# Performance work log

Hardware: AMD Instinct MI355X
Metric: run time of the kernel (lower is better)

## Reference

```python
import jax, jax.numpy as jnp
import numpy as np

NUM_HEADS = 12

def setup_inputs() -> dict:
    key = jax.random.key(0)
    ks = jax.random.split(key, 9)
    B, N, C = 4, 1024, 768
    hd = C // NUM_HEADS  # 64
    return {
        "x": jax.random.normal(ks[0], (B, N, C), dtype=jnp.float32),
        "prev_attn": jax.random.uniform(ks[1], (B, NUM_HEADS, N, N), dtype=jnp.float32) / N,
        "qkv_w": jax.random.normal(ks[2], (3 * C, C), dtype=jnp.float32) * 0.02,
        "proj_w": jax.random.normal(ks[3], (C, C), dtype=jnp.float32) * 0.02,
        "proj_b": jax.random.normal(ks[4], (C,), dtype=jnp.float32) * 0.02,
        "bp_w1": jax.random.normal(ks[5], (hd // 2, 2 * hd), dtype=jnp.float32) * 0.02,
        "bp_b1": jax.random.normal(ks[6], (hd // 2,), dtype=jnp.float32) * 0.02,
        "bp_w2": jax.random.normal(ks[7], (3, hd // 2), dtype=jnp.float32) * 0.02,
        "bp_b2": jax.random.normal(ks[8], (3,), dtype=jnp.float32) * 0.02,
    }

def reference(x, prev_attn, qkv_w, proj_w, proj_b, bp_w1, bp_b1, bp_w2, bp_b2):
    B, N, C = x.shape
    H = NUM_HEADS
    hd = C // H
    scale = hd ** -0.5
    # qkv projection: [B,N,3C] -> [3,B,H,N,hd]
    qkv = (x @ qkv_w.T).reshape(B, N, 3, H, hd).transpose(2, 0, 3, 1, 4)
    q, k, v = qkv[0], qkv[1], qkv[2]
    # scaled dot-product scores [B,H,N,N]
    attn_logits = jnp.einsum('bhnd,bhmd->bhnm', q, k) * scale
    cur_attn = jax.nn.softmax(attn_logits, axis=-1)
    # per-(b,h,n) bias MLP on concat(q,k): [B,H,N,2*hd] -> [B,H,N,3]
    qk = jnp.concatenate((q, k), axis=-1)
    h1 = jax.nn.relu(jnp.einsum('bhnd,od->bhno', qk, bp_w1) + bp_b1)
    bias = jnp.abs(jnp.einsum('bhno,po->bhnp', h1, bp_w2) + bp_b2)  # [B,H,N,3]
    # blend current attention, previous attention, and uniform term
    attn = (cur_attn * (1.0 + bias[..., 0:1])
            + prev_attn * bias[..., 1:2]
            - bias[..., 2:3] / N)
    out = jnp.einsum('bhnm,bhmd->bhnd', attn, v)  # [B,H,N,hd]
    out = out.transpose(0, 2, 1, 3).reshape(B, N, C)
    out = out @ proj_w.T + proj_b
    return (out, cur_attn)
```

## Files before the change

kernel.cpp:

```cpp
#include <hip/hip_runtime.h>

typedef __bf16 bf16_t;
typedef __bf16 bf16x8 __attribute__((ext_vector_type(8)));
typedef __bf16 bf16x4 __attribute__((ext_vector_type(4)));
typedef float f32x4 __attribute__((ext_vector_type(4)));

static constexpr int Bb = 4, Hh = 12, Nn = 1024, Cc = 768, HD = 64;
static constexpr int OUT0 = Bb * Nn * Cc;

#define GLD16(gp, lp)                                                       \
  __builtin_amdgcn_global_load_lds(                                         \
      (const __attribute__((address_space(1))) unsigned int*)(gp),          \
      (__attribute__((address_space(3))) unsigned int*)(lp), 16, 0, 0)

__global__ __launch_bounds__(256) void convert_all(
    const float* __restrict__ x, const float* __restrict__ qw, const float* __restrict__ pw,
    bf16_t* __restrict__ xb, bf16_t* __restrict__ qwb, bf16_t* __restrict__ pwb) {
  const int NX = (Bb * Nn * Cc) / 4;
  const int NQ = (3 * Cc * Cc) / 4;
  int i = blockIdx.x * 256 + threadIdx.x;
  const float4* src;
  bf16_t* dst;
  int off;
  if (i < NX) { src = (const float4*)x; dst = xb; off = i; }
  else if (i < NX + NQ) { src = (const float4*)qw; dst = qwb; off = i - NX; }
  else { src = (const float4*)pw; dst = pwb; off = i - NX - NQ; }
  float4 v = src[off];
  bf16x4 o;
  o[0] = (bf16_t)v.x; o[1] = (bf16_t)v.y; o[2] = (bf16_t)v.z; o[3] = (bf16_t)v.w;
  *(bf16x4*)(dst + (size_t)off * 4) = o;
}

__global__ __launch_bounds__(256) void gemm_qkv(
    const bf16_t* __restrict__ A, const bf16_t* __restrict__ Bm,
    bf16_t* __restrict__ q_bf, bf16_t* __restrict__ k_bf, bf16_t* __restrict__ vT_bf) {
  __shared__ bf16_t As[128 * 32];
  __shared__ bf16_t Bs[128 * 32];
  const int tid = threadIdx.x;
  const int lane = tid & 63;
  const int w = tid >> 6;
  const int wr = w >> 1, wc = w & 1;
  const int g = lane >> 4, r = lane & 15;
  const int m0 = (blockIdx.x / 18) << 7;
  const int n0 = (blockIdx.x % 18) << 7;

  const f32x4 fz = {0.f, 0.f, 0.f, 0.f};
  f32x4 acc[4][4];
#pragma unroll
  for (int i = 0; i < 4; i++)
#pragma unroll
    for (int j = 0; j < 4; j++) acc[i][j] = fz;

  for (int k0 = 0; k0 < 768; k0 += 32) {
#pragma unroll
    for (int c = 0; c < 2; c++) {
      int row = w * 32 + c * 16 + (lane >> 2);
      int kof = (lane & 3) << 3;
      GLD16(&A[(size_t)(m0 + row) * 768 + k0 + kof], (char*)As + w * 2048 + c * 1024);
      GLD16(&Bm[(size_t)(n0 + row) * 768 + k0 + kof], (char*)Bs + w * 2048 + c * 1024);
    }
    __syncthreads();
    bf16x8 af[4], bfv[4];
#pragma unroll
    for (int i = 0; i < 4; i++) af[i] = *(const bf16x8*)&As[(wr * 64 + i * 16 + r) * 32 + g * 8];
#pragma unroll
    for (int j = 0; j < 4; j++) bfv[j] = *(const bf16x8*)&Bs[(wc * 64 + j * 16 + r) * 32 + g * 8];
#pragma unroll
    for (int i = 0; i < 4; i++)
#pragma unroll
      for (int j = 0; j < 4; j++)
        acc[i][j] = __builtin_amdgcn_mfma_f32_16x16x32_bf16(af[i], bfv[j], acc[i][j], 0, 0, 0);
    __syncthreads();
  }

#pragma unroll
  for (int i = 0; i < 4; i++) {
#pragma unroll
    for (int j = 0; j < 4; j++) {
      int c = n0 + wc * 64 + j * 16 + r;
#pragma unroll
      for (int e = 0; e < 4; e++) {
        int mrow = m0 + wr * 64 + i * 16 + g * 4 + e;
        float val = acc[i][j][e];
        int which = c / 768;
        int cc = c - which * 768;
        int h = cc >> 6, d = cc & 63;
        int b = mrow >> 10, n = mrow & 1023;
        size_t bh = (size_t)(b * Hh + h);
        if (which == 0)      q_bf[(bh * Nn + n) * HD + d] = (bf16_t)val;
        else if (which == 1) k_bf[(bh * Nn + n) * HD + d] = (bf16_t)val;
        else                 vT_bf[(bh * HD + d) * Nn + n] = (bf16_t)val;
      }
    }
  }
}

__global__ __launch_bounds__(256) void gemm_proj64(
    const bf16_t* __restrict__ A, const bf16_t* __restrict__ Bm,
    float* __restrict__ outF, const float* __restrict__ bias) {
  __shared__ bf16_t As[64 * 40];
  __shared__ bf16_t Bs[128 * 40];
  const int tid = threadIdx.x, lane = tid & 63, w = tid >> 6;
  const int wr = w >> 1, wc = w & 1;
  const int g = lane >> 4, r = lane & 15;
  const int m0 = (blockIdx.x / 6) << 6;
  const int n0 = (blockIdx.x % 6) << 7;
  const f32x4 fz = {0.f, 0.f, 0.f, 0.f};
  f32x4 acc[2][4];
#pragma unroll
  for (int i = 0; i < 2; i++)
#pragma unroll
    for (int j = 0; j < 4; j++) acc[i][j] = fz;

  for (int k0 = 0; k0 < 768; k0 += 32) {
    {
      int row = tid >> 2, kof = (tid & 3) << 3;
      *(bf16x8*)&As[row * 40 + kof] = *(const bf16x8*)&A[(size_t)(m0 + row) * 768 + k0 + kof];
    }
#pragma unroll
    for (int p = 0; p < 2; p++) {
      int idx = tid + (p << 8);
      int row = idx >> 2, kof = (idx & 3) << 3;
      *(bf16x8*)&Bs[row * 40 + kof] = *(const bf16x8*)&Bm[(size_t)(n0 + row) * 768 + k0 + kof];
    }
    __syncthreads();
    bf16x8 af[2], bfv[4];
#pragma unroll
    for (int i = 0; i < 2; i++) af[i] = *(const bf16x8*)&As[(wr * 32 + i * 16 + r) * 40 + g * 8];
#pragma unroll
    for (int j = 0; j < 4; j++) bfv[j] = *(const bf16x8*)&Bs[(wc * 64 + j * 16 + r) * 40 + g * 8];
#pragma unroll
    for (int i = 0; i < 2; i++)
#pragma unroll
      for (int j = 0; j < 4; j++)
        acc[i][j] = __builtin_amdgcn_mfma_f32_16x16x32_bf16(af[i], bfv[j], acc[i][j], 0, 0, 0);
    __syncthreads();
  }

#pragma unroll
  for (int i = 0; i < 2; i++)
#pragma unroll
    for (int j = 0; j < 4; j++) {
      int c = n0 + wc * 64 + j * 16 + r;
#pragma unroll
      for (int e = 0; e < 4; e++) {
        int mrow = m0 + wr * 32 + i * 16 + g * 4 + e;
        outF[(size_t)mrow * 768 + c] = acc[i][j][e] + bias[c];
      }
    }
}

__global__ __launch_bounds__(256) void bias_mlp(
    const bf16_t* __restrict__ qb, const bf16_t* __restrict__ kb,
    const float* __restrict__ w1, const float* __restrict__ b1,
    const float* __restrict__ w2, const float* __restrict__ b2,
    float* __restrict__ bias4) {
  __shared__ float w1s[32 * 130];
  __shared__ float qks[8][128];
  __shared__ float h1s[8][32];
  const int t = threadIdx.x;
#pragma unroll
  for (int p = 0; p < 16; p++) {
    int idx = p * 256 + t;
    w1s[(idx >> 7) * 130 + (idx & 127)] = w1[idx];
  }
  const int rl = t >> 5, u = t & 31;
  const float b1u = b1[u];
  for (int ro = 0; ro < 4; ro++) {
    const int rowg = blockIdx.x * 32 + ro * 8 + rl;
    {
      int i4 = u * 4;
      const bf16_t* src = (i4 < 64) ? (qb + (size_t)rowg * HD + i4)
                                    : (kb + (size_t)rowg * HD + (i4 - 64));
      bf16x4 vv = *(const bf16x4*)src;
#pragma unroll
      for (int z = 0; z < 4; z++) qks[rl][i4 + z] = (float)vv[z];
    }
    __syncthreads();
    float accv = b1u;
#pragma unroll 16
    for (int i2 = 0; i2 < 64; i2++) {
      float2 wv = *(const float2*)&w1s[u * 130 + i2 * 2];
      float2 qv = *(const float2*)&qks[rl][i2 * 2];
      accv += wv.x * qv.x + wv.y * qv.y;
    }
    h1s[rl][u] = fmaxf(accv, 0.f);
    __syncthreads();
    if (u < 4) {
      float outv = 0.f;
      if (u < 3) {
        float s = b2[u];
#pragma unroll
        for (int j = 0; j < 32; j++) s += w2[u * 32 + j] * h1s[rl][j];
        float v = fabsf(s);
        outv = (u == 0) ? (1.f + v) : ((u == 1) ? v : -v * (1.f / (float)Nn));
      }
      bias4[(size_t)rowg * 4 + u] = outv;
    }
    __syncthreads();
  }
}

__global__ __launch_bounds__(256, 2) void attn_fused(
    const bf16_t* __restrict__ qb, const bf16_t* __restrict__ kb,
    const bf16_t* __restrict__ vT, const float* __restrict__ prev,
    const float* __restrict__ bias4, float* __restrict__ cur,
    bf16_t* __restrict__ oh) {
  __shared__ char Plb[32 * 2048];
  __shared__ float redsum[32][4];
  const int bid = blockIdx.x;
  const int tile = (bid & 7) * 192 + (bid >> 3);
  const int bh = tile >> 5, mt = tile & 31;
  const int tid = threadIdx.x;
  const int lane = tid & 63, w = tid >> 6;
  const int g = lane >> 4, r = lane & 15;
  const int row0 = mt << 5;
  const int cbase = w << 8;

  const bf16_t* qp = qb + ((size_t)bh * Nn + row0) * HD;
  const bf16_t* kp = kb + (size_t)bh * Nn * HD;
  const float* ppr0 = prev + (size_t)bh * Nn * Nn + (size_t)(row0 + r) * Nn + cbase + (g << 2);
  char* myPrev = Plb + (w << 14);
  bf16x8 q00 = *(const bf16x8*)&qp[r * HD + g * 8];
  bf16x8 q01 = *(const bf16x8*)&qp[r * HD + g * 8 + 32];
  bf16x8 q10 = *(const bf16x8*)&qp[(16 + r) * HD + g * 8];
  bf16x8 q11 = *(const bf16x8*)&qp[(16 + r) * HD + g * 8 + 32];
  bf16x8 qa0, qa1, qb0, qb1;
#pragma unroll
  for (int j = 0; j < 8; j++) {
    qa0[j] = (bf16_t)((float)q00[j] * 0.125f);
    qa1[j] = (bf16_t)((float)q01[j] * 0.125f);
    qb0[j] = (bf16_t)((float)q10[j] * 0.125f);
    qb1[j] = (bf16_t)((float)q11[j] * 0.125f);
  }
  const f32x4 fz = {0.f, 0.f, 0.f, 0.f};
  f32x4 acc0[16], acc1[16];
#pragma unroll
  for (int t = 0; t < 16; t++) {
    GLD16(ppr0 + (t << 4), myPrev + (t << 10));
    int col = cbase + (t << 4) + r;
    bf16x8 kf0 = *(const bf16x8*)&kp[(size_t)col * HD + g * 8];
    bf16x8 kf1 = *(const bf16x8*)&kp[(size_t)col * HD + g * 8 + 32];
    f32x4 z0 = __builtin_amdgcn_mfma_f32_16x16x32_bf16(kf0, qa0, fz, 0, 0, 0);
    acc0[t] = __builtin_amdgcn_mfma_f32_16x16x32_bf16(kf1, qa1, z0, 0, 0, 0);
    f32x4 z1 = __builtin_amdgcn_mfma_f32_16x16x32_bf16(kf0, qb0, fz, 0, 0, 0);
    acc1[t] = __builtin_amdgcn_mfma_f32_16x16x32_bf16(kf1, qb1, z1, 0, 0, 0);
  }

  float sj0 = 0.f, sj1 = 0.f;
  bf16x4 p0[16], p1[16];
#pragma unroll
  for (int t = 0; t < 16; t++) {
    float a0 = __expf(fminf(acc0[t][0], 30.f)), a1 = __expf(fminf(acc0[t][1], 30.f));
    float a2 = __expf(fminf(acc0[t][2], 30.f)), a3 = __expf(fminf(acc0[t][3], 30.f));
    sj0 += (a0 + a1) + (a2 + a3);
    p0[t][0] = (bf16_t)a0; p0[t][1] = (bf16_t)a1;
    p0[t][2] = (bf16_t)a2; p0[t][3] = (bf16_t)a3;
    float b0v = __expf(fminf(acc1[t][0], 30.f)), b1v = __expf(fminf(acc1[t][1], 30.f));
    float b2v = __expf(fminf(acc1[t][2], 30.f)), b3v = __expf(fminf(acc1[t][3], 30.f));
    sj1 += (b0v + b1v) + (b2v + b3v);
    p1[t][0] = (bf16_t)b0v; p1[t][1] = (bf16_t)b1v;
    p1[t][2] = (bf16_t)b2v; p1[t][3] = (bf16_t)b3v;
  }
  sj0 += __shfl_xor(sj0, 16, 64);
  sj0 += __shfl_xor(sj0, 32, 64);
  sj1 += __shfl_xor(sj1, 16, 64);
  sj1 += __shfl_xor(sj1, 32, 64);
  if (lane < 16) {
    redsum[lane][w] = sj0;
    redsum[16 + lane][w] = sj1;
  }
  __syncthreads();
  const float inv0 =
      1.f / (redsum[r][0] + redsum[r][1] + redsum[r][2] + redsum[r][3]);
  const float inv1 =
      1.f / (redsum[16 + r][0] + redsum[16 + r][1] + redsum[16 + r][2] + redsum[16 + r][3]);

  const float4 bv0 = *(const float4*)&bias4[((size_t)bh * 1024 + row0 + r) * 4];
  const float4 bv1 = *(const float4*)&bias4[((size_t)bh * 1024 + row0 + 16 + r) * 4];
  bf16x4 nb0[16];
#pragma unroll
  for (int t = 0; t < 16; t++) {
    f32x4 pvv = *(const f32x4*)(myPrev + (t << 10) + (lane << 4));
    nb0[t][0] = (bf16_t)(bv0.x * ((float)p0[t][0] * inv0) + bv0.y * pvv[0] + bv0.z);
    nb0[t][1] = (bf16_t)(bv0.x * ((float)p0[t][1] * inv0) + bv0.y * pvv[1] + bv0.z);
    nb0[t][2] = (bf16_t)(bv0.x * ((float)p0[t][2] * inv0) + bv0.y * pvv[2] + bv0.z);
    nb0[t][3] = (bf16_t)(bv0.x * ((float)p0[t][3] * inv0) + bv0.y * pvv[3] + bv0.z);
  }
  __syncthreads();

#pragma unroll
  for (int t = 0; t < 16; t++) {
    int col = cbase + (t << 4) + (g << 2);
    int off = (r * 2048 + col * 2) ^ ((r & 7) << 4);
    *(bf16x4*)(Plb + off) = nb0[t];
  }
  {
    const float* ppr = prev + (size_t)bh * Nn * Nn + (size_t)(row0 + 16 + r) * Nn + cbase + (g << 2);
#pragma unroll
    for (int t = 0; t < 16; t++) {
      float4 pvv = *(const float4*)&ppr[t << 4];
      bf16x4 nb;
      nb[0] = (bf16_t)(bv1.x * ((float)p1[t][0] * inv1) + bv1.y * pvv.x + bv1.z);
      nb[1] = (bf16_t)(bv1.x * ((float)p1[t][1] * inv1) + bv1.y * pvv.y + bv1.z);
      nb[2] = (bf16_t)(bv1.x * ((float)p1[t][2] * inv1) + bv1.y * pvv.z + bv1.z);
      nb[3] = (bf16_t)(bv1.x * ((float)p1[t][3] * inv1) + bv1.y * pvv.w + bv1.z);
      int col = cbase + (t << 4) + (g << 2);
      int off = ((16 + r) * 2048 + col * 2) ^ ((r & 7) << 4);
      *(bf16x4*)(Plb + off) = nb;
    }
  }
  __syncthreads();

  const bf16_t* vrow = vT + (size_t)bh * HD * Nn + (size_t)((w << 4) + r) * Nn;
  float* cp0 = cur + (size_t)bh * Nn * Nn + (size_t)(row0 + r) * Nn + cbase + (g << 2);
  float* cp1 = cur + (size_t)bh * Nn * Nn + (size_t)(row0 + 16 + r) * Nn + cbase + (g << 2);
  f32x4 o0q0 = fz, o0q1 = fz, o0q2 = fz, o0q3 = fz;
  f32x4 o1q0 = fz, o1q1 = fz, o1q2 = fz, o1q3 = fz;
#pragma unroll
  for (int ks = 0; ks < 8; ks++) {
    int kA = ks << 5;
#pragma unroll
    for (int q = 0; q < 4; q++) {
      int i = ks * 4 + q;
      if (i < 16) {
        float4 p;
        p.x = (float)p0[i][0] * inv0;
        p.y = (float)p0[i][1] * inv0;
        p.z = (float)p0[i][2] * inv0;
        p.w = (float)p0[i][3] * inv0;
        *(float4*)&cp0[i << 4] = p;
      } else {
        int t = i - 16;
        float4 p;
        p.x = (float)p1[t][0] * inv1;
        p.y = (float)p1[t][1] * inv1;
        p.z = (float)p1[t][2] * inv1;
        p.w = (float)p1[t][3] * inv1;
        *(float4*)&cp1[t << 4] = p;
      }
      int k0 = (q << 8) + kA;
      bf16x8 vb = *(const bf16x8*)&vrow[k0 + g * 8];
      bf16x8 pa0 = *(const bf16x8*)(Plb + ((r * 2048 + (k0 + g * 8) * 2) ^ ((r & 7) << 4)));
      bf16x8 pa1 = *(const bf16x8*)(Plb + (((16 + r) * 2048 + (k0 + g * 8) * 2) ^ ((r & 7) << 4)));
      if (q == 0) {
        o0q0 = __builtin_amdgcn_mfma_f32_16x16x32_bf16(pa0, vb, o0q0, 0, 0, 0);
        o1q0 = __builtin_amdgcn_mfma_f32_16x16x32_bf16(pa1, vb, o1q0, 0, 0, 0);
      } else if (q == 1) {
        o0q1 = __builtin_amdgcn_mfma_f32_16x16x32_bf16(pa0, vb, o0q1, 0, 0, 0);
        o1q1 = __builtin_amdgcn_mfma_f32_16x16x32_bf16(pa1, vb, o1q1, 0, 0, 0);
      } else if (q == 2) {
        o0q2 = __builtin_amdgcn_mfma_f32_16x16x32_bf16(pa0, vb, o0q2, 0, 0, 0);
        o1q2 = __builtin_amdgcn_mfma_f32_16x16x32_bf16(pa1, vb, o1q2, 0, 0, 0);
      } else {
        o0q3 = __builtin_amdgcn_mfma_f32_16x16x32_bf16(pa0, vb, o0q3, 0, 0, 0);
        o1q3 = __builtin_amdgcn_mfma_f32_16x16x32_bf16(pa1, vb, o1q3, 0, 0, 0);
      }
    }
  }
  f32x4 os0 = (o0q0 + o0q1) + (o0q2 + o0q3);
  f32x4 os1 = (o1q0 + o1q1) + (o1q2 + o1q3);
  const int b = bh / Hh, h = bh % Hh;
#pragma unroll
  for (int e = 0; e < 4; e++) {
    int nrow = row0 + g * 4 + e;
    oh[((size_t)(b * Nn + nrow)) * Cc + h * HD + (w << 4) + r] = (bf16_t)os0[e];
    oh[((size_t)(b * Nn + nrow + 16)) * Cc + h * HD + (w << 4) + r] = (bf16_t)os1[e];
  }
}

extern "C" void kernel_launch(void* const* d_in, const int* in_sizes, int n_in,
                              void* d_out, int out_size, void* d_ws, size_t ws_size,
                              hipStream_t stream) {
  const float* x      = (const float*)d_in[0];
  const float* prev   = (const float*)d_in[1];
  const float* qkv_w  = (const float*)d_in[2];
  const float* proj_w = (const float*)d_in[3];
  const float* proj_b = (const float*)d_in[4];
  const float* bp_w1  = (const float*)d_in[5];
  const float* bp_b1  = (const float*)d_in[6];
  const float* bp_w2  = (const float*)d_in[7];
  const float* bp_w2b = (const float*)d_in[8];

  float* out0 = (float*)d_out;
  float* cur  = out0 + OUT0;

  char* ws = (char*)d_ws;
  bf16_t* xb    = (bf16_t*)(ws + 0);
  bf16_t* qwb   = (bf16_t*)(ws + 6291456);
  bf16_t* pwb   = (bf16_t*)(ws + 9830400);
  bf16_t* qbf   = (bf16_t*)(ws + 11010048);
  bf16_t* kbf   = (bf16_t*)(ws + 17301504);
  bf16_t* vtb   = (bf16_t*)(ws + 23592960);
  float*  bias4 = (float*)(ws + 29884416);
  bf16_t* ohb   = (bf16_t*)(ws + 30670848);
  if (ws_size < 36962304) return;

  convert_all<<<5376, 256, 0, stream>>>(x, qkv_w, proj_w, xb, qwb, pwb);
  gemm_qkv<<<32 * 18, 256, 0, stream>>>(xb, qwb, qbf, kbf, vtb);
  bias_mlp<<<1536, 256, 0, stream>>>(qbf, kbf, bp_w1, bp_b1, bp_w2, bp_w2b, bias4);
  attn_fused<<<1536, 256, 0, stream>>>(qbf, kbf, vtb, prev, bias4, cur, ohb);
  gemm_proj64<<<64 * 6, 256, 0, stream>>>(ohb, pwb, out0, proj_b);
}
```

Baseline: 210.9 us.

## Split PV into two halves and overlap second prev_attn load via LDS staging

The attention kernel now runs the P·V MFMA for the first 16 rows before building the second half's blended probabilities, with that half's prev_attn rows loaded asynchronously into an LDS staging area (global_load_lds) in two chunks, overlapping the load with compute. The full __syncthreads calls are replaced with explicit waitcnt plus s_barrier. Separately, both GEMM kernels remap block IDs so consecutive blocks are spread across XCD groups, aiming for better L2 locality. In exchange the PV loop is serialized into two passes, adding an extra barrier and a second read of V from memory.

```diff
diff --git a/kernel.cpp b/kernel.cpp
--- a/kernel.cpp
+++ b/kernel.cpp
@@ -41,8 +41,9 @@
   const int w = tid >> 6;
   const int wr = w >> 1, wc = w & 1;
   const int g = lane >> 4, r = lane & 15;
-  const int m0 = (blockIdx.x / 18) << 7;
-  const int n0 = (blockIdx.x % 18) << 7;
+  const int bid2 = (blockIdx.x & 7) * 72 + (blockIdx.x >> 3);
+  const int m0 = (bid2 / 18) << 7;
+  const int n0 = (bid2 % 18) << 7;
 
   const f32x4 fz = {0.f, 0.f, 0.f, 0.f};
   f32x4 acc[4][4];
@@ -103,8 +104,9 @@
   const int tid = threadIdx.x, lane = tid & 63, w = tid >> 6;
   const int wr = w >> 1, wc = w & 1;
   const int g = lane >> 4, r = lane & 15;
-  const int m0 = (blockIdx.x / 6) << 6;
-  const int n0 = (blockIdx.x % 6) << 7;
+  const int bid2 = (blockIdx.x & 7) * 48 + (blockIdx.x >> 3);
+  const int m0 = (bid2 / 6) << 6;
+  const int n0 = (bid2 % 6) << 7;
   const f32x4 fz = {0.f, 0.f, 0.f, 0.f};
   f32x4 acc[2][4];
 #pragma unroll
@@ -220,7 +222,9 @@
   const bf16_t* qp = qb + ((size_t)bh * Nn + row0) * HD;
   const bf16_t* kp = kb + (size_t)bh * Nn * HD;
   const float* ppr0 = prev + (size_t)bh * Nn * Nn + (size_t)(row0 + r) * Nn + cbase + (g << 2);
+  const float* ppr1 = prev + (size_t)bh * Nn * Nn + (size_t)(row0 + 16 + r) * Nn + cbase + (g << 2);
   char* myPrev = Plb + (w << 14);
+  char* stg = Plb + 32768 + (w << 13);
   bf16x8 q00 = *(const bf16x8*)&qp[r * HD + g * 8];
   bf16x8 q01 = *(const bf16x8*)&qp[r * HD + g * 8 + 32];
   bf16x8 q10 = *(const bf16x8*)&qp[(16 + r) * HD + g * 8];
@@ -290,36 +294,23 @@
   __syncthreads();
 
 #pragma unroll
+  for (int t = 0; t < 8; t++) GLD16(ppr1 + (t << 4), stg + (t << 10));
+#pragma unroll
   for (int t = 0; t < 16; t++) {
     int col = cbase + (t << 4) + (g << 2);
     int off = (r * 2048 + col * 2) ^ ((r & 7) << 4);
     *(bf16x4*)(Plb + off) = nb0[t];
   }
-  {
-    const float* ppr = prev + (size_t)bh * Nn * Nn + (size_t)(row0 + 16 + r) * Nn + cbase + (g << 2);
-#pragma unroll
-    for (int t = 0; t < 16; t++) {
-      float4 pvv = *(const float4*)&ppr[t << 4];
-      bf16x4 nb;
-      nb[0] = (bf16_t)(bv1.x * ((float)p1[t][0] * inv1) + bv1.y * pvv.x + bv1.z);
-      nb[1] = (bf16_t)(bv1.x * ((float)p1[t][1] * inv1) + bv1.y * pvv.y + bv1.z);
-      nb[2] = (bf16_t)(bv1.x * ((float)p1[t][2] * inv1) + bv1.y * pvv.z + bv1.z);
-      nb[3] = (bf16_t)(bv1.x * ((float)p1[t][3] * inv1) + bv1.y * pvv.w + bv1.z);
-      int col = cbase + (t << 4) + (g << 2);
-      int off = ((16 + r) * 2048 + col * 2) ^ ((r & 7) << 4);
-      *(bf16x4*)(Plb + off) = nb;
-    }
-  }
-  __syncthreads();
+  asm volatile("s_waitcnt lgkmcnt(0)" ::: "memory");
+  __builtin_amdgcn_sched_barrier(0);
+  __builtin_amdgcn_s_barrier();
 
   const bf16_t* vrow = vT + (size_t)bh * HD * Nn + (size_t)((w << 4) + r) * Nn;
   float* cp0 = cur + (size_t)bh * Nn * Nn + (size_t)(row0 + r) * Nn + cbase + (g << 2);
   float* cp1 = cur + (size_t)bh * Nn * Nn + (size_t)(row0 + 16 + r) * Nn + cbase + (g << 2);
   f32x4 o0q0 = fz, o0q1 = fz, o0q2 = fz, o0q3 = fz;
-  f32x4 o1q0 = fz, o1q1 = fz, o1q2 = fz, o1q3 = fz;
 #pragma unroll
   for (int ks = 0; ks < 8; ks++) {
-    int kA = ks << 5;
 #pragma unroll
     for (int q = 0; q < 4; q++) {
       int i = ks * 4 + q;
@@ -330,35 +321,83 @@
         p.z = (float)p0[i][2] * inv0;
         p.w = (float)p0[i][3] * inv0;
         *(float4*)&cp0[i << 4] = p;
-      } else {
-        int t = i - 16;
-        float4 p;
-        p.x = (float)p1[t][0] * inv1;
-        p.y = (float)p1[t][1] * inv1;
-        p.z = (float)p1[t][2] * inv1;
-        p.w = (float)p1[t][3] * inv1;
-        *(float4*)&cp1[t << 4] = p;
       }
-      int k0 = (q << 8) + kA;
+      int k0 = (q << 8) + (ks << 5);
       bf16x8 vb = *(const bf16x8*)&vrow[k0 + g * 8];
       bf16x8 pa0 = *(const bf16x8*)(Plb + ((r * 2048 + (k0 + g * 8) * 2) ^ ((r & 7) << 4)));
+      if (q == 0) o0q0 = __builtin_amdgcn_mfma_f32_16x16x32_bf16(pa0, vb, o0q0, 0, 0, 0);
+      else if (q == 1) o0q1 = __builtin_amdgcn_mfma_f32_16x16x32_bf16(pa0, vb, o0q1, 0, 0, 0);
+      else if (q == 2) o0q2 = __builtin_amdgcn_mfma_f32_16x16x32_bf16(pa0, vb, o0q2, 0, 0, 0);
+      else o0q3 = __builtin_amdgcn_mfma_f32_16x16x32_bf16(pa0, vb, o0q3, 0, 0, 0);
+    }
+  }
+  f32x4 os0 = (o0q0 + o0q1) + (o0q2 + o0q3);
+
+  asm volatile("s_waitcnt vmcnt(0)" ::: "memory");
+  __builtin_amdgcn_sched_barrier(0);
+  f32x4 pvv0[8];
+#pragma unroll
+  for (int t = 0; t < 8; t++)
+    pvv0[t] = *(const f32x4*)(stg + (t << 10) + (lane << 4));
+  asm volatile("s_waitcnt lgkmcnt(0)" ::: "memory");
+  __builtin_amdgcn_sched_barrier(0);
+#pragma unroll
+  for (int t = 0; t < 8; t++) GLD16(ppr1 + ((t + 8) << 4), stg + (t << 10));
+  bf16x4 nb1[16];
+#pragma unroll
+  for (int t = 0; t < 8; t++) {
+    nb1[t][0] = (bf16_t)(bv1.x * ((float)p1[t][0] * inv1) + bv1.y * pvv0[t][0] + bv1.z);
+    nb1[t][1] = (bf16_t)(bv1.x * ((float)p1[t][1] * inv1) + bv1.y * pvv0[t][1] + bv1.z);
+    nb1[t][2] = (bf16_t)(bv1.x * ((float)p1[t][2] * inv1) + bv1.y * pvv0[t][2] + bv1.z);
+    nb1[t][3] = (bf16_t)(bv1.x * ((float)p1[t][3] * inv1) + bv1.y * pvv0[t][3] + bv1.z);
+  }
+  asm volatile("s_waitcnt vmcnt(0)" ::: "memory");
+  __builtin_amdgcn_sched_barrier(0);
+#pragma unroll
+  for (int t = 8; t < 16; t++) {
+    f32x4 pvv = *(const f32x4*)(stg + ((t - 8) << 10) + (lane << 4));
+    nb1[t][0] = (bf16_t)(bv1.x * ((float)p1[t][0] * inv1) + bv1.y * pvv[0] + bv1.z);
+    nb1[t][1] = (bf16_t)(bv1.x * ((float)p1[t][1] * inv1) + bv1.y * pvv[1] + bv1.z);
+    nb1[t][2] = (bf16_t)(bv1.x * ((float)p1[t][2] * inv1) + bv1.y * pvv[2] + bv1.z);
+    nb1[t][3] = (bf16_t)(bv1.x * ((float)p1[t][3] * inv1) + bv1.y * pvv[3] + bv1.z);
+  }
+  asm volatile("s_waitcnt lgkmcnt(0)" ::: "memory");
+  __builtin_amdgcn_sched_barrier(0);
+  __builtin_amdgcn_s_barrier();
+
+#pragma unroll
+  for (int t = 0; t < 16; t++) {
+    int col = cbase + (t << 4) + (g << 2);
+    int off = ((16 + r) * 2048 + col * 2) ^ ((r & 7) << 4);
+    *(bf16x4*)(Plb + off) = nb1[t];
+  }
+  asm volatile("s_waitcnt lgkmcnt(0)" ::: "memory");
+  __builtin_amdgcn_sched_barrier(0);
+  __builtin_amdgcn_s_barrier();
+
+  f32x4 o1q0 = fz, o1q1 = fz, o1q2 = fz, o1q3 = fz;
+#pragma unroll
+  for (int ks = 0; ks < 8; ks++) {
+#pragma unroll
+    for (int q = 0; q < 4; q++) {
+      int i = ks * 4 + q;
+      if (i < 16) {
+        float4 p;
+        p.x = (float)p1[i][0] * inv1;
+        p.y = (float)p1[i][1] * inv1;
+        p.z = (float)p1[i][2] * inv1;
+        p.w = (float)p1[i][3] * inv1;
+        *(float4*)&cp1[i << 4] = p;
+      }
+      int k0 = (q << 8) + (ks << 5);
+      bf16x8 vb = *(const bf16x8*)&vrow[k0 + g * 8];
       bf16x8 pa1 = *(const bf16x8*)(Plb + (((16 + r) * 2048 + (k0 + g * 8) * 2) ^ ((r & 7) << 4)));
-      if (q == 0) {
-        o0q0 = __builtin_amdgcn_mfma_f32_16x16x32_bf16(pa0, vb, o0q0, 0, 0, 0);
-        o1q0 = __builtin_amdgcn_mfma_f32_16x16x32_bf16(pa1, vb, o1q0, 0, 0, 0);
-      } else if (q == 1) {
-        o0q1 = __builtin_amdgcn_mfma_f32_16x16x32_bf16(pa0, vb, o0q1, 0, 0, 0);
-        o1q1 = __builtin_amdgcn_mfma_f32_16x16x32_bf16(pa1, vb, o1q1, 0, 0, 0);
-      } else if (q == 2) {
-        o0q2 = __builtin_amdgcn_mfma_f32_16x16x32_bf16(pa0, vb, o0q2, 0, 0, 0);
-        o1q2 = __builtin_amdgcn_mfma_f32_16x16x32_bf16(pa1, vb, o1q2, 0, 0, 0);
-      } else {
-        o0q3 = __builtin_amdgcn_mfma_f32_16x16x32_bf16(pa0, vb, o0q3, 0, 0, 0);
-        o1q3 = __builtin_amdgcn_mfma_f32_16x16x32_bf16(pa1, vb, o1q3, 0, 0, 0);
-      }
-    }
-  }
-  f32x4 os0 = (o0q0 + o0q1) + (o0q2 + o0q3);
+      if (q == 0) o1q0 = __builtin_amdgcn_mfma_f32_16x16x32_bf16(pa1, vb, o1q0, 0, 0, 0);
+      else if (q == 1) o1q1 = __builtin_amdgcn_mfma_f32_16x16x32_bf16(pa1, vb, o1q1, 0, 0, 0);
+      else if (q == 2) o1q2 = __builtin_amdgcn_mfma_f32_16x16x32_bf16(pa1, vb, o1q2, 0, 0, 0);
+      else o1q3 = __builtin_amdgcn_mfma_f32_16x16x32_bf16(pa1, vb, o1q3, 0, 0, 0);
+    }
+  }
   f32x4 os1 = (o1q0 + o1q1) + (o1q2 + o1q3);
   const int b = bh / Hh, h = bh % Hh;
 #pragma unroll
```

New measurement: 227.4 us. 7.8% more time.
